# Optimization experiments

Measured on AMD Instinct MI355X. Metric: run time of the kernel, lower is better.

The kernel has to match this reference:

```python
import jax, jax.numpy as jnp
import numpy as np

B, S, C_IN, D, H = 16, 1024, 1280, 512, 8
HD = D // H  # head dim = 64
EPS = 1e-5


def _rope(x):
    # x: [b, h, s, d]; half-split rotation as in the torch module
    d = x.shape[-1]
    half = d // 2
    s = x.shape[2]
    inv_freq = 1.0 / (10000.0 ** (jnp.arange(0, d, 2, dtype=jnp.float32) / d))  # [half]
    ang = jnp.arange(s, dtype=jnp.float32)[:, None] * inv_freq[None, :]  # [s, half]
    sin, cos = jnp.sin(ang), jnp.cos(ang)  # broadcast over [b, h]
    x1, x2 = x[..., :half], x[..., half:]
    return jnp.concatenate([x1 * cos - x2 * sin, x1 * sin + x2 * cos], axis=-1)


def _ln(x, g, b):
    mu = jnp.mean(x, axis=-1, keepdims=True)
    var = jnp.mean((x - mu) ** 2, axis=-1, keepdims=True)
    return (x - mu) * jax.lax.rsqrt(var + EPS) * g + b


def setup_inputs() -> dict:
    key = jax.random.key(0)
    ks = jax.random.split(key, 12)
    def lin(k, fan_in, fan_out):
        lim = 1.0 / np.sqrt(fan_in)
        return jax.random.uniform(k, (fan_in, fan_out), jnp.float32, -lim, lim)
    return {
        "x": jax.random.normal(ks[0], (B, S, C_IN), jnp.float32),
        "w_in": lin(ks[1], C_IN, D), "b_in": jnp.zeros((D,), jnp.float32),
        "w_qkv": lin(ks[2], D, 3 * D), "b_qkv": jnp.zeros((3 * D,), jnp.float32),
        "w_out": lin(ks[3], D, D), "b_out": jnp.zeros((D,), jnp.float32),
        "w_ffn1": lin(ks[4], D, 4 * D), "b_ffn1": jnp.zeros((4 * D,), jnp.float32),
        "w_ffn2": lin(ks[5], 4 * D, D), "b_ffn2": jnp.zeros((D,), jnp.float32),
        "g1": jnp.ones((D,), jnp.float32), "bn1": jnp.zeros((D,), jnp.float32),
        "g2": jnp.ones((D,), jnp.float32), "bn2": jnp.zeros((D,), jnp.float32),
    }


def reference(x, w_in, b_in, w_qkv, b_qkv, w_out, b_out,
              w_ffn1, b_ffn1, w_ffn2, b_ffn2, g1, bn1, g2, bn2):
    h = x @ w_in + b_in  # [b, s, D]
    qkv = (h @ w_qkv + b_qkv).reshape(B, S, 3, H, HD)
    q, k, v = (jnp.transpose(qkv[:, :, i], (0, 2, 1, 3)) for i in range(3))  # [b, h, s, d]
    q, k = _rope(q), _rope(k)
    scores = jnp.einsum('bhqd,bhkd->bhqk', q, k) / np.sqrt(HD)
    attn = jax.nn.softmax(scores, axis=-1)
    o = jnp.einsum('bhqk,bhkd->bhqd', attn, v)
    o = jnp.transpose(o, (0, 2, 1, 3)).reshape(B, S, D)
    o = o @ w_out + b_out
    h = _ln(h + o, g1, bn1)
    ffn = jax.nn.relu(h @ w_ffn1 + b_ffn1) @ w_ffn2 + b_ffn2
    return _ln(h + ffn, g2, bn2)
```

## Files before the change

kernel.cpp:

```cpp
#include <hip/hip_runtime.h>
#include <hip/hip_bf16.h>
#include <math.h>

#define B_   16
#define S_   1024
#define CIN  1280
#define D_   512
#define H_   8
#define HD_  64
#define NROW (B_ * S_)

typedef __bf16 bf16;
typedef float  f32x2  __attribute__((ext_vector_type(2)));
typedef float  f32x4  __attribute__((ext_vector_type(4)));
typedef bf16   bf16x4 __attribute__((ext_vector_type(4)));
typedef bf16   bf16x8 __attribute__((ext_vector_type(8)));

__device__ __forceinline__ void gload_lds16(const bf16* g, bf16* l) {
    __builtin_amdgcn_global_load_lds(
        (const __attribute__((address_space(1))) void*)g,
        (__attribute__((address_space(3))) void*)l, 16, 0, 0);
}

#define SBAR()   __builtin_amdgcn_s_barrier()
#define SCHED0() __builtin_amdgcn_sched_barrier(0)
#define VMCNT8() asm volatile("s_waitcnt vmcnt(8)" ::: "memory")
#define VMCNT2() asm volatile("s_waitcnt vmcnt(2)" ::: "memory")
#define VMCNT0() asm volatile("s_waitcnt vmcnt(0)" ::: "memory")

__device__ __forceinline__ void tr_tile(const float* __restrict__ in,
                                        bf16* __restrict__ out,
                                        int R, int C, int cx, int ry, int t)
{
    __shared__ float T[32][33];
    const int r0 = ry << 5, c0 = cx << 5;
    {
        int lr = t >> 3, lc = (t & 7) << 2;
        f32x4 v = *(const f32x4*)(in + (size_t)(r0 + lr) * C + c0 + lc);
        T[lr][lc] = v[0]; T[lr][lc + 1] = v[1]; T[lr][lc + 2] = v[2]; T[lr][lc + 3] = v[3];
    }
    __syncthreads();
    {
        int oc = t >> 3, orr = (t & 7) << 2;
        bf16x4 o;
        o[0] = (bf16)T[orr][oc];     o[1] = (bf16)T[orr + 1][oc];
        o[2] = (bf16)T[orr + 2][oc]; o[3] = (bf16)T[orr + 3][oc];
        *(bf16x4*)(out + (size_t)(c0 + oc) * R + r0 + orr) = o;
    }
}

#define NCVT (NROW * CIN / 4 / 256)

__global__ __launch_bounds__(256)
void prep_kernel(const float* __restrict__ x, bf16* __restrict__ x_b,
                 const float* __restrict__ w_in,   bf16* __restrict__ win_t,
                 const float* __restrict__ w_qkv,  bf16* __restrict__ wqkv_t,
                 const float* __restrict__ w_out,  bf16* __restrict__ wout_t,
                 const float* __restrict__ w_ffn1, bf16* __restrict__ wf1_t,
                 const float* __restrict__ w_ffn2, bf16* __restrict__ wf2_t,
                 float* __restrict__ cs)
{
    const int t   = threadIdx.x;
    int bid = blockIdx.x;
    if (bid < NCVT) {
        int i = bid * 256 + t;
        f32x4 v = *(const f32x4*)(x + (size_t)i * 4);
        bf16x4 o;
        o[0] = (bf16)v[0]; o[1] = (bf16)v[1]; o[2] = (bf16)v[2]; o[3] = (bf16)v[3];
        *(bf16x4*)(x_b + (size_t)i * 4) = o;
        return;
    }
    bid -= NCVT;
    if (bid < 640)  { tr_tile(w_in,   win_t,  1280, 512,  bid % 16, bid / 16, t); return; }
    bid -= 640;
    if (bid < 768)  { tr_tile(w_qkv,  wqkv_t, 512,  1536, bid % 48, bid / 48, t); return; }
    bid -= 768;
    if (bid < 256)  { tr_tile(w_out,  wout_t, 512,  512,  bid % 16, bid / 16, t); return; }
    bid -= 256;
    if (bid < 1024) { tr_tile(w_ffn1, wf1_t,  512,  2048, bid % 64, bid / 64, t); return; }
    bid -= 1024;
    if (bid < 1024) { tr_tile(w_ffn2, wf2_t,  2048, 512,  bid % 16, bid / 16, t); return; }
    bid -= 1024;
    {
        int idx = bid * 256 + t;
        int s = idx >> 5, i = idx & 31;
        float freq = exp2f(-(float)i * (13.287712379549449f / 32.f));
        float sn, c;
        sincosf((float)s * freq, &sn, &c);
        cs[(size_t)idx * 2]     = c;
        cs[(size_t)idx * 2 + 1] = sn;
    }
}
#define NPREP (NCVT + 640 + 768 + 256 + 1024 + 1024 + 128)

#define ASZ1 (128 * 64)

template<int EPI, bool RELU, bool RES, bool OUTF, bool OUTB>
__global__ __launch_bounds__(256, 2)
void gemm128_kernel(const bf16* __restrict__ A, const bf16* __restrict__ Wt,
                    const float* __restrict__ bias, const bf16* __restrict__ res,
                    float* __restrict__ outf, bf16* __restrict__ outb,
                    const float* __restrict__ cs, bf16* __restrict__ vt,
                    int M, int N, int K)
{
    __shared__ bf16 lds[4 * ASZ1];

    const int tid  = threadIdx.x;
    const int lane = tid & 63;
    const int wid  = tid >> 6;

    const int perX = (M >> 7) >> 3;
    const int lin  = blockIdx.x;
    const int idx  = lin >> 3;
    const int my   = (lin & 7) * perX + (idx & (perX - 1));
    const int nx   = idx / perX;
    const int m0   = my << 7, n0 = nx << 7;

    const int sRow = lane >> 3;
    const int sK   = ((lane & 7) ^ sRow) << 3;

    const int r2  = wid >> 1;
    const int c2  = wid & 1;
    const int cc  = lane & 15;
    const int g   = (lane >> 4) & 3;
    const int swz = (cc & 7) << 4;

    f32x4 acc[4][4] = {};

    auto stage = [&](int t, int b) {
        const bf16* gA = A  + (size_t)m0 * K + t * 64;
        const bf16* gB = Wt + (size_t)n0 * K + t * 64;
        bf16* lA = lds + b * ASZ1;
        bf16* lB = lds + 2 * ASZ1 + b * ASZ1;
        #pragma unroll
        for (int v = 0; v < 4; ++v) {
            const int ch = v * 4 + wid;
            gload_lds16(gA + (size_t)(ch * 8 + sRow) * K + sK, lA + ch * 512);
            gload_lds16(gB + (size_t)(ch * 8 + sRow) * K + sK, lB + ch * 512);
        }
    };

    const int T = K >> 6;
    stage(0, 0);
    stage(1, 1);
    VMCNT8();
    SCHED0();
    SBAR();

    for (int t = 0; t < T; ++t) {
        const int b = t & 1;
        const char* lA = (const char*)(lds + b * ASZ1);
        const char* lB = (const char*)(lds + 2 * ASZ1 + b * ASZ1);

        #pragma unroll
        for (int ks = 0; ks < 2; ++ks) {
            bf16x8 af[4], bfr[4];
            #pragma unroll
            for (int i = 0; i < 4; ++i) {
                const int row = r2 * 64 + i * 16 + cc;
                af[i] = *(const bf16x8*)(lA + row * 128 + ((ks * 64 + g * 16) ^ swz));
            }
            #pragma unroll
            for (int j = 0; j < 4; ++j) {
                const int row = c2 * 64 + j * 16 + cc;
                bfr[j] = *(const bf16x8*)(lB + row * 128 + ((ks * 64 + g * 16) ^ swz));
            }
            __builtin_amdgcn_s_setprio(1);
            #pragma unroll
            for (int i = 0; i < 4; ++i)
                #pragma unroll
                for (int j = 0; j < 4; ++j)
                    acc[i][j] = __builtin_amdgcn_mfma_f32_16x16x32_bf16(af[i], bfr[j], acc[i][j], 0, 0, 0);
            __builtin_amdgcn_s_setprio(0);
        }
        SCHED0();
        SBAR();
        if (t + 2 < T) {
            stage(t + 2, b);
            VMCNT8();
        } else if (t + 1 < T) {
            VMCNT0();
        }
        if (t + 1 < T) { SCHED0(); SBAR(); }
    }

    const int rq = g << 2;
    if constexpr (EPI == 1) {
        const int colb = c2 * 64;
        if (nx < 8) {
            float bj[4];
            #pragma unroll
            for (int j = 0; j < 4; ++j) bj[j] = bias[n0 + colb + j * 16 + cc];
            #pragma unroll
            for (int i = 0; i < 4; ++i) {
                #pragma unroll
                for (int r = 0; r < 4; ++r) {
                    const int gm = m0 + r2 * 64 + i * 16 + rq + r;
                    const int s  = gm & (S_ - 1);
                    #pragma unroll
                    for (int jp = 0; jp < 2; ++jp) {
                        const int d = jp * 16 + cc;
                        f32x2 csv = *(const f32x2*)(cs + ((size_t)s * 32 + d) * 2);
                        float x1 = acc[i][jp][r]     + bj[jp];
                        float x2 = acc[i][jp + 2][r] + bj[jp + 2];
                        const size_t o1 = (size_t)gm * N + n0 + colb + d;
                        outb[o1]      = (bf16)(x1 * csv[0] - x2 * csv[1]);
                        outb[o1 + 32] = (bf16)(x1 * csv[1] + x2 * csv[0]);
                    }
                }
            }
        } else {
            const int col0 = n0 + colb;
            const int hw = (col0 >> 6) & 7;
            const int bb = m0 >> 10;
            bf16* vbase = vt + (size_t)(bb * 8 + hw) * (HD_ * S_);
            const int sb0 = (m0 & (S_ - 1)) + r2 * 64 + rq;
            #pragma unroll
            for (int i = 0; i < 4; ++i) {
                #pragma unroll
                for (int j = 0; j < 4; ++j) {
                    const int d = j * 16 + cc;
                    const float bv = bias[col0 + d];
                    bf16x4 pk;
                    #pragma unroll
                    for (int r = 0; r < 4; ++r) pk[r] = (bf16)(acc[i][j][r] + bv);
                    *(bf16x4*)(vbase + (size_t)d * S_ + sb0 + i * 16) = pk;
                }
            }
        }
    } else {
        #pragma unroll
        for (int i = 0; i < 4; ++i) {
            #pragma unroll
            for (int j = 0; j < 4; ++j) {
                const int gn = n0 + c2 * 64 + j * 16 + cc;
                const float bv = bias[gn];
                #pragma unroll
                for (int r = 0; r < 4; ++r) {
                    const int gm = m0 + r2 * 64 + i * 16 + rq + r;
                    float v = acc[i][j][r] + bv;
                    if (RES)  v += (float)res[(size_t)gm * N + gn];
                    if (RELU) v = fmaxf(v, 0.f);
                    if (OUTF) outf[(size_t)gm * N + gn] = v;
                    if (OUTB) outb[(size_t)gm * N + gn] = (bf16)v;
                }
            }
        }
    }
    (void)cs; (void)vt;
}

#define PST 72

__global__ __launch_bounds__(512)
void attn_kernel(const bf16* __restrict__ qkv, const bf16* __restrict__ vtg,
                 bf16* __restrict__ o)
{
    __shared__ bf16 Ks[2][4096];
    __shared__ bf16 Vs[2][4096];
    __shared__ bf16 Ps[8][16 * PST];

    const int bh  = blockIdx.x;
    const int b   = bh >> 3;
    const int h   = bh & 7;
    const int q0  = blockIdx.y << 7;
    const int tid = threadIdx.x;
    const int lane = tid & 63;
    const int w    = tid >> 6;
    const int c    = lane & 15;
    const int g    = lane >> 4;
    const int swz  = (c & 7) << 4;

    const size_t rs = 3 * D_;
    const bf16* qb = qkv + (size_t)b * S_ * rs + h * HD_;
    const bf16* kb = qb + D_;
    const bf16* vt = vtg + (size_t)bh * HD_ * S_;

    const int sRow = tid >> 3;
    const int sOff = ((tid & 7) ^ (sRow & 7)) << 3;

    bf16x8 qf[2];
    {
        const bf16* qrow = qb + (size_t)(q0 + w * 16 + c) * rs + g * 8;
        qf[0] = *(const bf16x8*)(qrow);
        qf[1] = *(const bf16x8*)(qrow + 32);
    }
    SCHED0();

    bf16x8 vones;
    {
        bf16 one = (bf16)(c == 0 ? 1.f : 0.f);
        #pragma unroll
        for (int u = 0; u < 8; ++u) vones[u] = one;
    }

    auto stage = [&](int t, int buf) {
        gload_lds16(kb + (size_t)(t * 64 + sRow) * rs + sOff, &Ks[buf][0] + (size_t)tid * 8);
        gload_lds16(vt + (size_t)sRow * S_ + t * 64 + sOff,   &Vs[buf][0] + (size_t)tid * 8);
    };

    f32x4 oa[4] = {};
    f32x4 oa5 = {};
    float m_r = -3.0e38f;
    const float CE  = 0.18033688011112042f;
    const float THR = 44.3614195558365f;

    stage(0, 0);
    stage(1, 1);
    VMCNT2();
    SCHED0();
    SBAR();

    for (int t = 0; t < 16; ++t) {
        const int buf = t & 1;
        const char* kB = (const char*)Ks[buf];
        const char* vB = (const char*)Vs[buf];

        f32x4 sa[4] = {};
        __builtin_amdgcn_s_setprio(1);
        #pragma unroll
        for (int ch = 0; ch < 2; ++ch)
            #pragma unroll
            for (int ks = 0; ks < 4; ++ks) {
                bf16x8 kf = *(const bf16x8*)(kB + (ks * 16 + c) * 128 + ((ch * 64 + g * 16) ^ swz));
                sa[ks] = __builtin_amdgcn_mfma_f32_16x16x32_bf16(kf, qf[ch], sa[ks], 0, 0, 0);
            }
        __builtin_amdgcn_s_setprio(0);

        float pmax = -3.0e38f;
        #pragma unroll
        for (int ks = 0; ks < 4; ++ks)
            pmax = fmaxf(pmax, fmaxf(fmaxf(sa[ks][0], sa[ks][1]), fmaxf(sa[ks][2], sa[ks][3])));
        pmax = fmaxf(pmax, __shfl_xor(pmax, 16, 64));
        pmax = fmaxf(pmax, __shfl_xor(pmax, 32, 64));

        if (!__all(pmax - m_r <= THR)) {
            float mnew = fmaxf(m_r, pmax);
            float sc = __builtin_amdgcn_exp2f((m_r - mnew) * CE);
            #pragma unroll
            for (int r = 0; r < 4; ++r) {
                float scr = __shfl(sc, g * 4 + r, 64);
                #pragma unroll
                for (int j = 0; j < 4; ++j) oa[j][r] *= scr;
                oa5[r] *= scr;
            }
            m_r = mnew;
        }

        const float nmCE = -m_r * CE;
        #pragma unroll
        for (int ks = 0; ks < 4; ++ks) {
            bf16x4 pb;
            #pragma unroll
            for (int r = 0; r < 4; ++r)
                pb[r] = (bf16)__builtin_amdgcn_exp2f(__builtin_fmaf(sa[ks][r], CE, nmCE));
            *(bf16x4*)&Ps[w][c * PST + ks * 16 + g * 4] = pb;
        }

        __builtin_amdgcn_s_setprio(1);
        #pragma unroll
        for (int ch = 0; ch < 2; ++ch) {
            bf16x8 pa = *(const bf16x8*)&Ps[w][c * PST + ch * 32 + g * 8];
            #pragma unroll
            for (int j = 0; j < 4; ++j) {
                bf16x8 vf = *(const bf16x8*)(vB + (j * 16 + c) * 128 + ((ch * 64 + g * 16) ^ swz));
                oa[j] = __builtin_amdgcn_mfma_f32_16x16x32_bf16(pa, vf, oa[j], 0, 0, 0);
            }
            oa5 = __builtin_amdgcn_mfma_f32_16x16x32_bf16(pa, vones, oa5, 0, 0, 0);
        }
        __builtin_amdgcn_s_setprio(0);

        SCHED0();
        SBAR();
        if (t + 2 < 16) {
            stage(t + 2, buf);
            VMCNT2();
        } else if (t + 1 < 16) {
            VMCNT0();
        }
        if (t + 1 < 16) { SCHED0(); SBAR(); }
    }

    float linv[4];
    #pragma unroll
    for (int r = 0; r < 4; ++r)
        linv[r] = 1.f / __shfl(oa5[r], lane & 48, 64);
    #pragma unroll
    for (int j = 0; j < 4; ++j)
        #pragma unroll
        for (int r = 0; r < 4; ++r) {
            int q = q0 + w * 16 + g * 4 + r;
            o[((size_t)(b * S_) + q) * D_ + h * HD_ + j * 16 + c] = (bf16)(oa[j][r] * linv[r]);
        }
}

template<bool OUTF, bool OUTB>
__global__ __launch_bounds__(256)
void ln_kernel(const float* __restrict__ in, const float* __restrict__ g,
               const float* __restrict__ be, float* __restrict__ outf,
               bf16* __restrict__ outb)
{
    const int row  = (blockIdx.x << 2) + (threadIdx.x >> 6);
    const int lane = threadIdx.x & 63;
    const float* p = in + (size_t)row * D_;
    f32x4 a  = *(const f32x4*)(p + lane * 4);
    f32x4 b2 = *(const f32x4*)(p + 256 + lane * 4);
    float s  = a[0] + a[1] + a[2] + a[3] + b2[0] + b2[1] + b2[2] + b2[3];
    float s2 = a[0]*a[0] + a[1]*a[1] + a[2]*a[2] + a[3]*a[3]
             + b2[0]*b2[0] + b2[1]*b2[1] + b2[2]*b2[2] + b2[3]*b2[3];
    #pragma unroll
    for (int off = 32; off; off >>= 1) {
        s  += __shfl_xor(s,  off, 64);
        s2 += __shfl_xor(s2, off, 64);
    }
    const float mean = s * (1.f / 512.f);
    const float var  = s2 * (1.f / 512.f) - mean * mean;
    const float rstd = rsqrtf(var + 1e-5f);

    f32x4 g0 = *(const f32x4*)(g + lane * 4);
    f32x4 g1 = *(const f32x4*)(g + 256 + lane * 4);
    f32x4 e0 = *(const f32x4*)(be + lane * 4);
    f32x4 e1 = *(const f32x4*)(be + 256 + lane * 4);
    f32x4 o0, o1;
    #pragma unroll
    for (int u = 0; u < 4; u++) {
        o0[u] = (a[u]  - mean) * rstd * g0[u] + e0[u];
        o1[u] = (b2[u] - mean) * rstd * g1[u] + e1[u];
    }
    if (OUTF) {
        float* of = outf + (size_t)row * D_;
        *(f32x4*)(of + lane * 4)       = o0;
        *(f32x4*)(of + 256 + lane * 4) = o1;
    }
    if (OUTB) {
        bf16x4 c0, c1;
        #pragma unroll
        for (int u = 0; u < 4; u++) { c0[u] = (bf16)o0[u]; c1[u] = (bf16)o1[u]; }
        bf16* ob = outb + (size_t)row * D_;
        *(bf16x4*)(ob + lane * 4)       = c0;
        *(bf16x4*)(ob + 256 + lane * 4) = c1;
    }
}

extern "C" void kernel_launch(void* const* d_in, const int* in_sizes, int n_in,
                              void* d_out, int out_size, void* d_ws, size_t ws_size,
                              hipStream_t stream)
{
    const float* x      = (const float*)d_in[0];
    const float* w_in   = (const float*)d_in[1];
    const float* b_in   = (const float*)d_in[2];
    const float* w_qkv  = (const float*)d_in[3];
    const float* b_qkv  = (const float*)d_in[4];
    const float* w_out  = (const float*)d_in[5];
    const float* b_out  = (const float*)d_in[6];
    const float* w_ffn1 = (const float*)d_in[7];
    const float* b_ffn1 = (const float*)d_in[8];
    const float* w_ffn2 = (const float*)d_in[9];
    const float* b_ffn2 = (const float*)d_in[10];
    const float* g1     = (const float*)d_in[11];
    const float* bn1    = (const float*)d_in[12];
    const float* g2     = (const float*)d_in[13];
    const float* bn2    = (const float*)d_in[14];

    char* ws = (char*)d_ws;
    constexpr size_t OFF_XB   = 0;
    constexpr size_t OFF_WIN  = OFF_XB   + 41943040ull;
    constexpr size_t OFF_WQKV = OFF_WIN  + 1310720ull;
    constexpr size_t OFF_WOUT = OFF_WQKV + 1572864ull;
    constexpr size_t OFF_WF1  = OFF_WOUT + 524288ull;
    constexpr size_t OFF_WF2  = OFF_WF1  + 2097152ull;
    constexpr size_t OFF_CS   = OFF_WF2  + 2097152ull;
    constexpr size_t OFF_HB   = OFF_CS   + 33554432ull;
    constexpr size_t OFF_QKV  = OFF_HB   + 16777216ull;
    constexpr size_t OFF_OB   = OFF_QKV  + 50331648ull;
    constexpr size_t OFF_VT   = OFF_OB   + 16777216ull;
    constexpr size_t OFF_H2B  = OFF_VT   + 33554432ull;
    constexpr size_t OFF_F1   = OFF_H2B  + 16777216ull;
    constexpr size_t OFF_T1   = OFF_XB;
    constexpr size_t OFF_T2   = OFF_QKV;

    bf16*  x_b    = (bf16*)(ws + OFF_XB);
    bf16*  win_t  = (bf16*)(ws + OFF_WIN);
    bf16*  wqkv_t = (bf16*)(ws + OFF_WQKV);
    bf16*  wout_t = (bf16*)(ws + OFF_WOUT);
    bf16*  wf1_t  = (bf16*)(ws + OFF_WF1);
    bf16*  wf2_t  = (bf16*)(ws + OFF_WF2);
    float* cs_t   = (float*)(ws + OFF_CS);
    bf16*  h_b    = (bf16*)(ws + OFF_HB);
    bf16*  qkv_b  = (bf16*)(ws + OFF_QKV);
    bf16*  o_b    = (bf16*)(ws + OFF_OB);
    bf16*  vt_g   = (bf16*)(ws + OFF_VT);
    bf16*  h2_b   = (bf16*)(ws + OFF_H2B);
    bf16*  f1_b   = (bf16*)(ws + OFF_F1);
    float* t1_f   = (float*)(ws + OFF_T1);
    float* t2_f   = (float*)(ws + OFF_T2);

    prep_kernel<<<NPREP, 256, 0, stream>>>(x, x_b, w_in, win_t, w_qkv, wqkv_t,
                                           w_out, wout_t, w_ffn1, wf1_t,
                                           w_ffn2, wf2_t, cs_t);

    gemm128_kernel<0,false,false,false,true><<<(NROW/128) * (D_/128), 256, 0, stream>>>(
        x_b, win_t, b_in, nullptr, nullptr, h_b, nullptr, nullptr, NROW, D_, CIN);
    gemm128_kernel<1,false,false,false,true><<<(NROW/128) * (3*D_/128), 256, 0, stream>>>(
        h_b, wqkv_t, b_qkv, nullptr, nullptr, qkv_b, cs_t, vt_g, NROW, 3*D_, D_);
    attn_kernel<<<dim3(B_*H_, S_/128), 512, 0, stream>>>(qkv_b, vt_g, o_b);
    gemm128_kernel<0,false,true,true,false><<<(NROW/128) * (D_/128), 256, 0, stream>>>(
        o_b, wout_t, b_out, h_b, t1_f, nullptr, nullptr, nullptr, NROW, D_, D_);
    ln_kernel<false,true><<<NROW/4, 256, 0, stream>>>(t1_f, g1, bn1, nullptr, h2_b);
    gemm128_kernel<0,true,false,false,true><<<(NROW/128) * (4*D_/128), 256, 0, stream>>>(
        h2_b, wf1_t, b_ffn1, nullptr, nullptr, f1_b, nullptr, nullptr, NROW, 4*D_, D_);
    gemm128_kernel<0,false,true,true,false><<<(NROW/128) * (D_/128), 256, 0, stream>>>(
        f1_b, wf2_t, b_ffn2, h2_b, t2_f, nullptr, nullptr, nullptr, NROW, D_, 4*D_);
    ln_kernel<true,false><<<NROW/4, 256, 0, stream>>>(t2_f, g2, bn2, (float*)d_out, nullptr);

    (void)in_sizes; (void)n_in; (void)out_size; (void)ws_size;
}
```

Before: 263.5 us.

## Triple-buffer attention K/V tiles and store pre-LayerNorm residuals in bf16

```diff
diff --git a/kernel.cpp b/kernel.cpp
--- a/kernel.cpp
+++ b/kernel.cpp
@@ -256,8 +256,8 @@
 void attn_kernel(const bf16* __restrict__ qkv, const bf16* __restrict__ vtg,
                  bf16* __restrict__ o)
 {
-    __shared__ bf16 Ks[2][4096];
-    __shared__ bf16 Vs[2][4096];
+    __shared__ bf16 Ks[3][4096];
+    __shared__ bf16 Vs[3][4096];
     __shared__ bf16 Ps[8][16 * PST];
 
     const int bh  = blockIdx.x;
@@ -312,9 +312,11 @@
     SBAR();
 
     for (int t = 0; t < 16; ++t) {
-        const int buf = t & 1;
-        const char* kB = (const char*)Ks[buf];
-        const char* vB = (const char*)Vs[buf];
+        const int buf = t % 3;
+        if (t + 2 < 16) stage(t + 2, (t + 2) % 3);
+
+        const char* kB = (const char*)&Ks[buf][0];
+        const char* vB = (const char*)&Vs[buf][0];
 
         f32x4 sa[4] = {};
         __builtin_amdgcn_s_setprio(1);
@@ -371,14 +373,10 @@
         __builtin_amdgcn_s_setprio(0);
 
         SCHED0();
-        SBAR();
-        if (t + 2 < 16) {
-            stage(t + 2, buf);
-            VMCNT2();
-        } else if (t + 1 < 16) {
-            VMCNT0();
-        }
-        if (t + 1 < 16) { SCHED0(); SBAR(); }
+        if (t + 1 < 16) {
+            if (t + 2 < 16) { VMCNT2(); } else { VMCNT0(); }
+            SBAR();
+        }
     }
 
     float linv[4];
@@ -396,18 +394,22 @@
 
 template<bool OUTF, bool OUTB>
 __global__ __launch_bounds__(256)
-void ln_kernel(const float* __restrict__ in, const float* __restrict__ g,
+void ln_kernel(const bf16* __restrict__ in, const float* __restrict__ g,
                const float* __restrict__ be, float* __restrict__ outf,
                bf16* __restrict__ outb)
 {
     const int row  = (blockIdx.x << 2) + (threadIdx.x >> 6);
     const int lane = threadIdx.x & 63;
-    const float* p = in + (size_t)row * D_;
-    f32x4 a  = *(const f32x4*)(p + lane * 4);
-    f32x4 b2 = *(const f32x4*)(p + 256 + lane * 4);
-    float s  = a[0] + a[1] + a[2] + a[3] + b2[0] + b2[1] + b2[2] + b2[3];
-    float s2 = a[0]*a[0] + a[1]*a[1] + a[2]*a[2] + a[3]*a[3]
-             + b2[0]*b2[0] + b2[1]*b2[1] + b2[2]*b2[2] + b2[3]*b2[3];
+    const bf16* p = in + (size_t)row * D_ + lane * 8;
+    bf16x8 raw = *(const bf16x8*)p;
+    float v[8];
+    float s = 0.f, s2 = 0.f;
+    #pragma unroll
+    for (int u = 0; u < 8; ++u) {
+        v[u] = (float)raw[u];
+        s  += v[u];
+        s2 += v[u] * v[u];
+    }
     #pragma unroll
     for (int off = 32; off; off >>= 1) {
         s  += __shfl_xor(s,  off, 64);
@@ -417,28 +419,29 @@
     const float var  = s2 * (1.f / 512.f) - mean * mean;
     const float rstd = rsqrtf(var + 1e-5f);
 
-    f32x4 g0 = *(const f32x4*)(g + lane * 4);
-    f32x4 g1 = *(const f32x4*)(g + 256 + lane * 4);
-    f32x4 e0 = *(const f32x4*)(be + lane * 4);
-    f32x4 e1 = *(const f32x4*)(be + 256 + lane * 4);
-    f32x4 o0, o1;
+    f32x4 g0 = *(const f32x4*)(g + lane * 8);
+    f32x4 g1 = *(const f32x4*)(g + lane * 8 + 4);
+    f32x4 e0 = *(const f32x4*)(be + lane * 8);
+    f32x4 e1 = *(const f32x4*)(be + lane * 8 + 4);
+    float ov[8];
     #pragma unroll
-    for (int u = 0; u < 4; u++) {
-        o0[u] = (a[u]  - mean) * rstd * g0[u] + e0[u];
-        o1[u] = (b2[u] - mean) * rstd * g1[u] + e1[u];
+    for (int u = 0; u < 4; ++u) {
+        ov[u]     = (v[u]     - mean) * rstd * g0[u] + e0[u];
+        ov[u + 4] = (v[u + 4] - mean) * rstd * g1[u] + e1[u];
     }
     if (OUTF) {
-        float* of = outf + (size_t)row * D_;
-        *(f32x4*)(of + lane * 4)       = o0;
-        *(f32x4*)(of + 256 + lane * 4) = o1;
+        float* of = outf + (size_t)row * D_ + lane * 8;
+        f32x4 o0, o1;
+        #pragma unroll
+        for (int u = 0; u < 4; ++u) { o0[u] = ov[u]; o1[u] = ov[u + 4]; }
+        *(f32x4*)(of)     = o0;
+        *(f32x4*)(of + 4) = o1;
     }
     if (OUTB) {
-        bf16x4 c0, c1;
-        #pragma unroll
-        for (int u = 0; u < 4; u++) { c0[u] = (bf16)o0[u]; c1[u] = (bf16)o1[u]; }
-        bf16* ob = outb + (size_t)row * D_;
-        *(bf16x4*)(ob + lane * 4)       = c0;
-        *(bf16x4*)(ob + 256 + lane * 4) = c1;
+        bf16x8 ob;
+        #pragma unroll
+        for (int u = 0; u < 8; ++u) ob[u] = (bf16)ov[u];
+        *(bf16x8*)(outb + (size_t)row * D_ + lane * 8) = ob;
     }
 }
 
@@ -492,8 +495,8 @@
     bf16*  vt_g   = (bf16*)(ws + OFF_VT);
     bf16*  h2_b   = (bf16*)(ws + OFF_H2B);
     bf16*  f1_b   = (bf16*)(ws + OFF_F1);
-    float* t1_f   = (float*)(ws + OFF_T1);
-    float* t2_f   = (float*)(ws + OFF_T2);
+    bf16*  t1_b   = (bf16*)(ws + OFF_T1);
+    bf16*  t2_b   = (bf16*)(ws + OFF_T2);
 
     prep_kernel<<<NPREP, 256, 0, stream>>>(x, x_b, w_in, win_t, w_qkv, wqkv_t,
                                            w_out, wout_t, w_ffn1, wf1_t,
@@ -504,14 +507,14 @@
     gemm128_kernel<1,false,false,false,true><<<(NROW/128) * (3*D_/128), 256, 0, stream>>>(
         h_b, wqkv_t, b_qkv, nullptr, nullptr, qkv_b, cs_t, vt_g, NROW, 3*D_, D_);
     attn_kernel<<<dim3(B_*H_, S_/128), 512, 0, stream>>>(qkv_b, vt_g, o_b);
-    gemm128_kernel<0,false,true,true,false><<<(NROW/128) * (D_/128), 256, 0, stream>>>(
-        o_b, wout_t, b_out, h_b, t1_f, nullptr, nullptr, nullptr, NROW, D_, D_);
-    ln_kernel<false,true><<<NROW/4, 256, 0, stream>>>(t1_f, g1, bn1, nullptr, h2_b);
+    gemm128_kernel<0,false,true,false,true><<<(NROW/128) * (D_/128), 256, 0, stream>>>(
+        o_b, wout_t, b_out, h_b, nullptr, t1_b, nullptr, nullptr, NROW, D_, D_);
+    ln_kernel<false,true><<<NROW/4, 256, 0, stream>>>(t1_b, g1, bn1, nullptr, h2_b);
     gemm128_kernel<0,true,false,false,true><<<(NROW/128) * (4*D_/128), 256, 0, stream>>>(
         h2_b, wf1_t, b_ffn1, nullptr, nullptr, f1_b, nullptr, nullptr, NROW, 4*D_, D_);
-    gemm128_kernel<0,false,true,true,false><<<(NROW/128) * (D_/128), 256, 0, stream>>>(
-        f1_b, wf2_t, b_ffn2, h2_b, t2_f, nullptr, nullptr, nullptr, NROW, D_, 4*D_);
-    ln_kernel<true,false><<<NROW/4, 256, 0, stream>>>(t2_f, g2, bn2, (float*)d_out, nullptr);
+    gemm128_kernel<0,false,true,false,true><<<(NROW/128) * (D_/128), 256, 0, stream>>>(
+        f1_b, wf2_t, b_ffn2, h2_b, nullptr, t2_b, nullptr, nullptr, NROW, D_, 4*D_);
+    ln_kernel<true,false><<<NROW/4, 256, 0, stream>>>(t2_b, g2, bn2, (float*)d_out, nullptr);
 
     (void)in_sizes; (void)n_in; (void)out_size; (void)ws_size;
 }
```

Result: no change. 258.4 us (-2.0%).
